# Optimization experiments

Hardware: AMD Instinct MI355X
Metric: run time of the kernel (lower is better)

Reference implementation:

```python
import jax, jax.numpy as jnp
import numpy as np

B, N, DIM = 4, 2048, 768
HEADS, DH, DEPTH = 12, 64, 4
W = 35                     # hard-coded window size
P = DIM // 2               # window-embedding proj dim
V4 = DIM // 4              # window-embedding value dim
PB = DIM // 4              # dynamic pos-bias MLP width
FF = DIM * 4
NEG = float(np.finfo(np.float32).max)


def setup_inputs() -> dict:
    key = jax.random.key(0)
    ks = iter(jax.random.split(key, 32))
    r = lambda shape: jax.random.normal(next(ks), shape, jnp.float32) * 0.02
    return dict(
        x=jax.random.normal(next(ks), (B, N, DIM), jnp.float32),
        mask=jnp.zeros((B, N), bool),
        ln1_g=jnp.ones((DEPTH, DIM)), ln1_b=jnp.zeros((DEPTH, DIM)),
        qkv_W=r((DEPTH, DIM, 3 * HEADS * DH)),
        temp=jnp.full((DEPTH,), 15.5, jnp.float32),
        we_lin_W=r((DEPTH, DIM, P)), we_q_W=r((DEPTH, P, P)),
        we_k_W=r((DEPTH, DIM, P)), we_v_W=r((DEPTH, DIM, V4)),
        we_bos=jnp.zeros((DEPTH, V4)), we_scale=jnp.ones((DEPTH,)),
        out_W=r((DEPTH, DIM + V4, DIM)),
        ln2_g=jnp.ones((DEPTH, DIM)), ln2_b=jnp.zeros((DEPTH, DIM)),
        glu_W=r((DEPTH, DIM, 2 * FF)), glu_b=jnp.zeros((DEPTH, 2 * FF)),
        ffo_W=r((DEPTH, FF, DIM)), ffo_b=jnp.zeros((DEPTH, DIM)),
        pb_W1=r((1, PB)), pb_b1=jnp.zeros((PB,)),
        pb_W2=r((PB, PB)), pb_b2=jnp.zeros((PB,)),
        pb_W3=r((PB, HEADS)), pb_b3=jnp.zeros((HEADS,)),
    )


def _ln(x, g, b):
    m = x.mean(-1, keepdims=True)
    v = ((x - m) ** 2).mean(-1, keepdims=True)
    return (x - m) * jax.lax.rsqrt(v + 1e-5) * g + b


def _l2norm(t):
    # matches F.normalize(p=2, dim=-1): x / max(||x||, 1e-12)
    return t / jnp.maximum(jnp.linalg.norm(t, axis=-1, keepdims=True), 1e-12)


def _pos_bias(n, W1, b1, W2, b2, W3, b3):
    # DynamicPositionBias(dim=PB, depth=2): Linear->ReLU, Linear->ReLU, Linear
    pos = jnp.arange(-n + 1, n, dtype=jnp.float32)[:, None]          # (2n-1, 1)
    h = jax.nn.relu(pos @ W1 + b1)
    h = jax.nn.relu(h @ W2 + b2)
    out = h @ W3 + b3                                                # (2n-1, H)
    idx = jnp.arange(n)[:, None] - jnp.arange(n)[None, :] + n - 1    # (n, n)
    return jnp.transpose(out[idx], (2, 0, 1))                        # (H, n, n)


def _sinu(n, scale):
    # ScaledSinuEmbedding over proj dim P
    inv = 1.0 / (10000.0 ** (jnp.arange(0, P, 2, dtype=jnp.float32) / P))
    s = jnp.arange(n, dtype=jnp.float32)[:, None] * inv[None, :]
    return jnp.concatenate([jnp.sin(s), jnp.cos(s)], -1) * scale     # (n, P)


def _forward(x, mask, ln1_g, ln1_b, qkv_W, temp, we_lin_W, we_q_W, we_k_W,
             we_v_W, we_bos, we_scale, out_W, ln2_g, ln2_b, glu_W, glu_b,
             ffo_W, ffo_b, pb_W1, pb_b1, pb_W2, pb_b2, pb_W3, pb_b3):
    Bz, Nn, _ = x.shape
    pad = (-Nn) % W
    nw = (Nn + pad) // W
    bias = _pos_bias(W, pb_W1, pb_b1, pb_W2, pb_b2, pb_W3, pb_b3)    # (H, W, W)
    causal = jnp.triu(jnp.ones((W, W), bool), 1)
    mpad = jnp.concatenate([mask, jnp.ones((Bz, pad), bool)], 1).reshape(Bz, nw, W)
    valid = ~mpad                                                    # (B, w, n)
    amask = ~(valid[:, None, :, :, None] & valid[:, None, :, None, :]) | causal
    we_mask = mpad[:, :, None, :]                                    # (B, w, 1, n)
    lengths = jnp.maximum(valid.sum(-1), 1).astype(jnp.float32)[..., None, None]
    sinu35 = _sinu(W, 1.0)                                           # (W, P)

    for l in range(DEPTH):
        # ---- PreNorm + windowed cosine attention ----
        h = _ln(x, ln1_g[l], ln1_b[l])
        hp = jnp.concatenate([h, jnp.zeros((Bz, pad, DIM), h.dtype)], 1)
        hp = hp.reshape(Bz, nw, W, DIM)
        qkv = (hp @ qkv_W[l]).reshape(Bz, nw, W, HEADS, DH, 3)
        q, k, v = (jnp.transpose(qkv[..., i], (0, 3, 1, 2, 4)) for i in range(3))
        q, k = _l2norm(q), _l2norm(k)
        dots = jnp.einsum('bhwid,bhwjd->bhwij', q, k) * temp[l] + bias[None, :, None]
        dots = jnp.where(amask, -NEG, dots)
        attn = jax.nn.softmax(dots, axis=-1)
        o = jnp.einsum('bhwij,bhwjd->bhwid', attn, v)
        o = jnp.transpose(o, (0, 2, 3, 1, 4)).reshape(Bz, nw, W, HEADS * DH)
        # ---- window_embeddings: pooled prev-window embedding attention ----
        we = jnp.where(mpad[..., None], 0.0, o) @ we_lin_W[l]         # (B,w,n,P)
        we = jax.nn.relu(we.sum(-2, keepdims=True) / lengths)        # (B,w,1,P)
        wq = we @ we_q_W[l]
        k2 = o @ we_k_W[l] + sinu35 * we_scale[l]
        v2 = o @ we_v_W[l]
        d2 = jnp.einsum('bwid,bwjd->bwij', wq, k2) * (P ** -0.5)
        d2 = jnp.where(we_mask, -NEG, d2)
        o2 = jnp.einsum('bwij,bwjd->bwid', jax.nn.softmax(d2, -1), v2)  # (B,w,1,V4)
        bos = jnp.broadcast_to(we_bos[l], (Bz, 1, 1, V4))
        o2 = jnp.concatenate([bos, o2], 1)[:, :-1]                   # shift by one window
        o = jnp.concatenate([o, jnp.broadcast_to(o2, (Bz, nw, W, V4))], -1)
        o = (o @ out_W[l]).reshape(Bz, nw * W, DIM)[:, :Nn]
        x = x + o
        # ---- PreNorm + GLU feed-forward ----
        h2 = _ln(x, ln2_g[l], ln2_b[l])
        a, g = jnp.split(h2 @ glu_W[l] + glu_b[l], 2, axis=-1)
        x = x + ((a * jax.nn.silu(g)) @ ffo_W[l] + ffo_b[l])
    return x


def reference(x, mask, ln1_g, ln1_b, qkv_W, temp, we_lin_W, we_q_W, we_k_W,
              we_v_W, we_bos, we_scale, out_W, ln2_g, ln2_b, glu_W, glu_b,
              ffo_W, ffo_b, pb_W1, pb_b1, pb_W2, pb_b2, pb_W3, pb_b3):
    return _forward(x, mask, ln1_g, ln1_b, qkv_W, temp, we_lin_W, we_q_W,
                    we_k_W, we_v_W, we_bos, we_scale, out_W, ln2_g, ln2_b,
                    glu_W, glu_b, ffo_W, ffo_b, pb_W1, pb_b1, pb_W2, pb_b2,
                    pb_W3, pb_b3)
```

## Files before the change

### kernel.cpp

```cpp
#include <hip/hip_runtime.h>
#include <hip/hip_bf16.h>
#include <cstddef>
#include <cstdint>

#define B_ 4
#define N_ 2048
#define DIM_ 768
#define HEADS_ 12
#define DH_ 64
#define DEPTH_ 4
#define W_ 35
#define P_ 384
#define V4_ 192
#define FF_ 3072
#define NW_ 59
#define NPB_ (NW_*W_)
#define NTOK_ (B_*N_)
#define NWB_ (B_*NW_)
#define NTP_ (NWB_*W_)
#define NTPA_ 8448
#define NEG_ 3.402823466e+38f
#define QLD_ 65

typedef __bf16 bf16x8 __attribute__((ext_vector_type(8)));
typedef float  f32x4  __attribute__((ext_vector_type(4)));

#define GLOAD16(g, l) __builtin_amdgcn_global_load_lds( \
    (const __attribute__((address_space(1))) uint32_t*)(g), \
    (__attribute__((address_space(3))) uint32_t*)(l), 16, 0, 0)


__global__ __launch_bounds__(192) void posbias1_k(
    const float* __restrict__ W1, const float* __restrict__ b1,
    const float* __restrict__ W2, const float* __restrict__ b2,
    const float* __restrict__ W3, const float* __restrict__ b3,
    float* __restrict__ outk)
{
    __shared__ float h1[192];
    __shared__ float h2[192];
    int i = blockIdx.x;
    int tid = threadIdx.x;
    float pos = (float)(i - 34);
    h1[tid] = fmaxf(pos*W1[tid] + b1[tid], 0.f);
    __syncthreads();
    float s = b2[tid];
    for (int k=0;k<192;k++) s += h1[k]*W2[k*192+tid];
    h2[tid] = fmaxf(s, 0.f);
    __syncthreads();
    if (tid < 12){
        float o = b3[tid];
        for (int k=0;k<192;k++) o += h2[k]*W3[k*12+tid];
        outk[i*12+tid] = o;
    }
}

__global__ void posbias2_k(const float* __restrict__ outk, float* __restrict__ bias)
{
    int e = threadIdx.x + blockIdx.x*blockDim.x;
    if (e >= HEADS_*W_*W_) return;
    int h=e/(W_*W_); int rem=e%(W_*W_); int i=rem/W_; int j=rem%W_;
    bias[e] = outk[(i-j+W_-1)*12 + h];
}

__global__ void sinu_k(float* __restrict__ sinu)
{
    int i = blockIdx.x;
    int k = threadIdx.x;
    float inv = powf(10000.f, -(float)k/192.f);
    float s = (float)i * inv;
    sinu[i*P_ + k]       = sinf(s);
    sinu[i*P_ + 192 + k] = cosf(s);
}

__global__ void len_k(const unsigned char* __restrict__ mask, float* __restrict__ len)
{
    int bw = threadIdx.x + blockIdx.x*blockDim.x;
    if (bw >= NWB_) return;
    int b = bw / NW_, w = bw % NW_;
    int cnt = 0;
    for (int t=0;t<W_;t++){
        int g = w*W_ + t;
        if (g < N_ && mask[b*N_+g]==0) cnt++;
    }
    len[bw] = fmaxf((float)cnt, 1.f);
}

__global__ __launch_bounds__(256) void bosproj_k(
    const float* __restrict__ bos, const float* __restrict__ outW,
    float* __restrict__ bosp)
{
    int l = blockIdx.y;
    int c = blockIdx.x*256 + threadIdx.x;
    if (c >= DIM_) return;
    const float* W2 = outW + (size_t)l*(DIM_+V4_)*DIM_ + (size_t)DIM_*DIM_;
    const float* bl = bos + (size_t)l*V4_;
    float s = 0;
    for (int k=0;k<V4_;k++) s += bl[k]*W2[(size_t)k*DIM_ + c];
    bosp[(size_t)l*DIM_ + c] = s;
}

__global__ __launch_bounds__(256) void pack_k(
    const float* __restrict__ W, __bf16* __restrict__ Bp,
    int N, int Ncov, int Nld, size_t lsW, size_t lsB, int qkvperm, int ncol0)
{
    int n = blockIdx.x*256 + threadIdx.x;
    int k8 = blockIdx.y, l = blockIdx.z;
    if (n >= Ncov) return;
    bf16x8 v;
    if (n < N){
        int sn = n;
        if (qkvperm){ int s = n/768, hd = n - s*768; sn = hd*3 + s; }
        const float* w = W + lsW*l + (size_t)k8*8*N + sn;
        #pragma unroll
        for (int e=0;e<8;e++) v[e] = (__bf16)w[(size_t)e*N];
    } else {
        #pragma unroll
        for (int e=0;e<8;e++) v[e] = (__bf16)0.f;
    }
    *(bf16x8*)(Bp + lsB*l + ((size_t)k8*Nld + ncol0 + n)*8) = v;
}

__global__ __launch_bounds__(256) void ln_k(
    const float* __restrict__ x, const float* __restrict__ g,
    const float* __restrict__ b, __bf16* __restrict__ out,
    const float* __restrict__ o2p, const float* __restrict__ bosp, int padded)
{
    int r = blockIdx.x;
    int tid = threadIdx.x;
    int lane = tid & 63, wave = tid >> 6;
    int row = r; bool real = true;
    if (padded){
        int bb = r / NPB_, n = r % NPB_;
        if (n >= N_) real = false;
        row = bb*N_ + n;
    }
    float v0=0,v1=0,v2=0;
    if (real){
        const float* xr = x + (size_t)row*DIM_;
        v0 = xr[tid]; v1 = xr[tid+256]; v2 = xr[tid+512];
        if (o2p){
            int bb = row / N_, nn = row % N_;
            int widx = nn / W_;
            const float* op = widx ? o2p + (size_t)(bb*NW_ + widx - 1)*DIM_
                                   : bosp;
            v0 += op[tid]; v1 += op[tid+256]; v2 += op[tid+512];
        }
    }
    float s1 = v0+v1+v2;
    float s2 = v0*v0+v1*v1+v2*v2;
    #pragma unroll
    for (int off=32; off; off>>=1){
        s1 += __shfl_xor(s1, off);
        s2 += __shfl_xor(s2, off);
    }
    __shared__ float a1[4], a2[4];
    if (lane==0){ a1[wave]=s1; a2[wave]=s2; }
    __syncthreads();
    s1 = a1[0]+a1[1]+a1[2]+a1[3];
    s2 = a2[0]+a2[1]+a2[2]+a2[3];
    float m   = s1 * (1.f/768.f);
    float var = s2 * (1.f/768.f) - m*m;
    float inv = rsqrtf(var + 1e-5f);
    __bf16* o = out + (size_t)r*DIM_;
    if (!real){ o[tid]=(__bf16)0.f; o[tid+256]=(__bf16)0.f; o[tid+512]=(__bf16)0.f; return; }
    o[tid]     = (__bf16)((v0-m)*inv*g[tid]     + b[tid]);
    o[tid+256] = (__bf16)((v1-m)*inv*g[tid+256] + b[tid+256]);
    o[tid+512] = (__bf16)((v2-m)*inv*g[tid+512] + b[tid+512]);
}

template<int EPI, bool DUAL, int BM>
__global__ __launch_bounds__(256) void mgemm_k(
    const __bf16* __restrict__ A, const __bf16* __restrict__ Bp,
    float* __restrict__ Cf, __bf16* __restrict__ Cb, float* __restrict__ Cf2,
    float* __restrict__ Cx,
    const float* __restrict__ bias, const float* __restrict__ extra,
    const float* __restrict__ scale_ptr,
    int M, int K, int Nc, int Nld, int Cld)
{
    constexpr int BN = DUAL ? 64 : 128;
    constexpr int RS = BM / 2;
    constexpr int MF = RS / 16;
    constexpr int NF = (BN/2) / 16;
    constexpr int AS = BM * 32;
    constexpr int BS = BN * 32;
    constexpr int ALD = BM / 64;
    constexpr int NL  = ALD + 2;
    __shared__ alignas(16) __bf16 As[3*AS];
    __shared__ alignas(16) __bf16 Bs[3*BS];
    __shared__ alignas(16) __bf16 Gs[DUAL ? 3*BS : 16];
    const int tid = threadIdx.x;
    const int lane = tid & 63, wave = tid >> 6;
    const int wr = wave >> 1, wc = wave & 1;
    const int m0 = blockIdx.y*BM;
    const int n0 = blockIdx.x*BN;
    const int lk = lane >> 4, lr = lane & 15;
    f32x4 acc[MF][NF] = {};
    f32x4 acc2[DUAL?MF:1][NF] = {};

    const __bf16* aP[ALD];
    int aO[ALD];
    #pragma unroll
    for (int q=0;q<ALD;q++){
        int i = tid + q*256;
        int r = i & (BM-1), k8 = i / BM;
        aP[q] = A + (size_t)(m0+r)*K + k8*8;
        aO[q] = i*8;
    }
    const __bf16* bP[2];
    int bO[2];
    if constexpr (!DUAL){
        #pragma unroll
        for (int q=0;q<2;q++){
            int i = tid + q*256;
            int n = i & 127, k8 = i >> 7;
            bP[q] = Bp + ((size_t)k8*Nld + n0 + n)*8;
            bO[q] = i*8;
        }
    } else {
        int n = tid & 63, k8 = tid >> 6;
        bP[0] = Bp + ((size_t)k8*Nld + n0 + n)*8;
        bP[1] = bP[0] + (size_t)FF_*8;
        bO[0] = tid*8;
        bO[1] = tid*8;
    }
    const size_t bStep = (size_t)Nld*32;

    auto stage = [&](int wb){
        #pragma unroll
        for (int q=0;q<ALD;q++)
            GLOAD16(aP[q], As + wb*AS + aO[q]);
        if constexpr (!DUAL){
            GLOAD16(bP[0], Bs + wb*BS + bO[0]);
            GLOAD16(bP[1], Bs + wb*BS + bO[1]);
        } else {
            GLOAD16(bP[0], Bs + wb*BS + bO[0]);
            GLOAD16(bP[1], Gs + wb*BS + bO[1]);
        }
        #pragma unroll
        for (int q=0;q<ALD;q++) aP[q] += 32;
        bP[0] += bStep; bP[1] += bStep;
    };

    const int nk = K >> 5;
    stage(0);
    stage(1);
    int rb = 0;
    for (int t = 0; t < nk; ++t){
        if (t == nk-1)              asm volatile("s_waitcnt vmcnt(0)" ::: "memory");
        else if constexpr (NL == 3) asm volatile("s_waitcnt vmcnt(3)" ::: "memory");
        else                        asm volatile("s_waitcnt vmcnt(4)" ::: "memory");
        __builtin_amdgcn_s_barrier();
        __builtin_amdgcn_sched_barrier(0);
        if (t + 2 < nk){
            int wb = rb + 2; if (wb >= 3) wb -= 3;
            stage(wb);
        }
        const __bf16* as = As + rb*AS + (size_t)(lk*BM + wr*RS + lr)*8;
        const __bf16* bs = Bs + rb*BS + (size_t)(lk*BN + wc*(BN/2) + lr)*8;
        bf16x8 af[MF], bfr[NF];
        #pragma unroll
        for (int m=0;m<MF;m++) af[m] = *(const bf16x8*)(as + m*128);
        #pragma unroll
        for (int n=0;n<NF;n++) bfr[n] = *(const bf16x8*)(bs + n*128);
        __builtin_amdgcn_s_setprio(1);
        #pragma unroll
        for (int m=0;m<MF;m++)
            #pragma unroll
            for (int n=0;n<NF;n++)
                acc[m][n] = __builtin_amdgcn_mfma_f32_16x16x32_bf16(af[m], bfr[n], acc[m][n], 0,0,0);
        if constexpr (DUAL){
            const __bf16* gs = Gs + rb*BS + (size_t)(lk*BN + wc*(BN/2) + lr)*8;
            bf16x8 gfr[NF];
            #pragma unroll
            for (int n=0;n<NF;n++) gfr[n] = *(const bf16x8*)(gs + n*128);
            #pragma unroll
            for (int m=0;m<MF;m++)
                #pragma unroll
                for (int n=0;n<NF;n++)
                    acc2[m][n] = __builtin_amdgcn_mfma_f32_16x16x32_bf16(af[m], gfr[n], acc2[m][n], 0,0,0);
        }
        __builtin_amdgcn_s_setprio(0);
        rb++; if (rb >= 3) rb = 0;
    }

    const int lq = lane >> 4;
    #pragma unroll
    for (int m=0;m<MF;m++){
        #pragma unroll
        for (int r=0;r<4;r++){
            int row = m0 + wr*RS + m*16 + lq*4 + r;
            if (row >= M) continue;
            #pragma unroll
            for (int n=0;n<NF;n++){
                int col = n0 + wc*(BN/2) + n*16 + lr;
                if (col >= Nc) continue;
                float v = acc[m][n][r];
                if (EPI==1){
                    Cb[(size_t)row*Cld + col] = (__bf16)v;
                } else if (EPI==3){
                    int bb = row / N_, nn = row % N_;
                    int widx = nn / W_;
                    const float* src = widx
                        ? extra + (size_t)(bb*NW_ + widx - 1)*DIM_
                        : scale_ptr;
                    Cf[(size_t)row*Cld + col] += v + bias[col] + src[col];
                } else if (EPI==4){
                    float a_ = v + bias[col];
                    float g_ = acc2[m][n][r] + bias[col + FF_];
                    Cb[(size_t)row*Cld + col] = (__bf16)(a_ * (g_ / (1.f + expf(-g_))));
                } else if (EPI==8){
                    if (col < P_){
                        int tt = (row % NPB_) % W_;
                        Cf[(size_t)row*P_ + col] = v + extra[tt*P_ + col]*scale_ptr[0];
                    } else if (col < 576){
                        Cf2[(size_t)row*V4_ + (col - P_)] = v;
                    } else {
                        int bb = row / NPB_, nn = row % NPB_;
                        if (nn < N_)
                            Cx[(size_t)(bb*N_ + nn)*DIM_ + (col - 576)] += v;
                    }
                }
            }
        }
    }
}

__global__ __launch_bounds__(256) void attn_k(
    const __bf16* __restrict__ qkv, const unsigned char* __restrict__ mask,
    const float* __restrict__ bias, const float* __restrict__ temp_p,
    __bf16* __restrict__ obuf, float* __restrict__ osum)
{
    int bid = blockIdx.x;
    int w = bid % NW_;
    int h = (bid / NW_) % HEADS_;
    int b = bid / (NW_*HEADS_);
    int tid = threadIdx.x;
    __shared__ float qs[W_*QLD_], ks[W_*QLD_], vs[W_*DH_];
    __shared__ float sc[W_*W_];
    __shared__ float osacc[4][64];
    __shared__ int vf[W_];
    int bw = b*NW_ + w;
    int rbase = bw*W_;
    for (int e=tid; e<W_*DH_; e+=256){
        int t=e>>6, d=e&63;
        size_t idx = (size_t)(rbase+t)*(3*DIM_) + h*DH_ + d;
        qs[t*QLD_+d]=(float)qkv[idx];
        ks[t*QLD_+d]=(float)qkv[idx+768];
        vs[e]=(float)qkv[idx+1536];
    }
    if (tid < W_){
        int g = w*W_ + tid;
        vf[tid] = (g < N_) && (mask[b*N_+g]==0);
    }
    __syncthreads();
    for (int e=tid; e<2*W_; e+=256){
        float* src = (e<W_)? qs : ks;
        int t = (e<W_)? e : e-W_;
        float s=0;
        for (int d=0;d<DH_;d++){ float v=src[t*QLD_+d]; s+=v*v; }
        float inv = 1.f / fmaxf(sqrtf(s), 1e-12f);
        for (int d=0;d<DH_;d++) src[t*QLD_+d] *= inv;
    }
    __syncthreads();
    float temp = temp_p[0];
    for (int e=tid; e<W_*W_; e+=256){
        int i=e/W_, j=e%W_;
        float s;
        if (!vf[i] || !vf[j] || j>i) s = -NEG_;
        else {
            float acc=0;
            for (int d=0;d<DH_;d++) acc += qs[i*QLD_+d]*ks[j*QLD_+d];
            s = acc*temp + bias[(h*W_+i)*W_+j];
        }
        sc[e]=s;
    }
    __syncthreads();
    if (tid < W_){
        int i=tid;
        float mx=-INFINITY;
        for (int j=0;j<W_;j++) mx=fmaxf(mx, sc[i*W_+j]);
        float sum=0;
        for (int j=0;j<W_;j++){ float e_=expf(sc[i*W_+j]-mx); sc[i*W_+j]=e_; sum+=e_; }
        float inv=1.f/sum;
        for (int j=0;j<W_;j++) sc[i*W_+j]*=inv;
    }
    __syncthreads();
    int wavei = tid >> 6, d = tid & 63;
    float psum = 0.f;
    for (int i = wavei; i < W_; i += 4){
        float s=0;
        for (int j=0;j<W_;j++) s += sc[i*W_+j]*vs[j*DH_+d];
        obuf[(size_t)(rbase+i)*DIM_ + h*DH_ + d] = (__bf16)s;
        if (vf[i]) psum += s;
    }
    osacc[wavei][d] = psum;
    __syncthreads();
    if (tid < 64)
        osum[(size_t)bw*DIM_ + h*DH_ + tid] =
            osacc[0][tid]+osacc[1][tid]+osacc[2][tid]+osacc[3][tid];
}

__global__ __launch_bounds__(384) void wefuse_k(
    const float* __restrict__ osum, const float* __restrict__ we_lin,
    const float* __restrict__ we_q, const float* __restrict__ k2,
    const float* __restrict__ v2, const unsigned char* __restrict__ mask,
    const float* __restrict__ len, const float* __restrict__ W2,
    float* __restrict__ o2p)
{
    int bw = blockIdx.x;
    int b = bw / NW_, w = bw % NW_;
    int tid = threadIdx.x;
    __shared__ float osr[768], werr[384], wqr[384], pp[W_], o2s[V4_];
    osr[tid]     = osum[(size_t)bw*DIM_ + tid];
    osr[tid+384] = osum[(size_t)bw*DIM_ + tid + 384];
    __syncthreads();
    float invlen = 1.f / len[bw];
    float s = 0;
    for (int k=0;k<768;k++) s += osr[k]*we_lin[(size_t)k*P_ + tid];
    werr[tid] = fmaxf(s*invlen, 0.f);
    __syncthreads();
    s = 0;
    for (int k=0;k<384;k++) s += werr[k]*we_q[(size_t)k*P_ + tid];
    wqr[tid] = s;
    __syncthreads();
    if (tid < W_){
        int g = w*W_ + tid;
        bool val = (g < N_) && (mask[b*N_+g]==0);
        float sv = -NEG_;
        if (val){
            float acc=0;
            const float* kr = k2 + (size_t)(bw*W_+tid)*P_;
            for (int c=0;c<P_;c++) acc += wqr[c]*kr[c];
            sv = acc * 0.05103103630798287f;
        }
        pp[tid]=sv;
    }
    __syncthreads();
    if (tid==0){
        float mx=-INFINITY;
        for (int j=0;j<W_;j++) mx=fmaxf(mx,pp[j]);
        float sum=0;
        for (int j=0;j<W_;j++){ float e=expf(pp[j]-mx); pp[j]=e; sum+=e; }
        float inv=1.f/sum;
        for (int j=0;j<W_;j++) pp[j]*=inv;
    }
    __syncthreads();
    if (tid < V4_){
        float sv=0;
        for (int j=0;j<W_;j++) sv += pp[j]*v2[(size_t)(bw*W_+j)*V4_ + tid];
        o2s[tid] = sv;
    }
    __syncthreads();
    #pragma unroll
    for (int c = tid; c < DIM_; c += 384){
        float s2 = 0;
        for (int k=0;k<V4_;k++) s2 += o2s[k]*W2[(size_t)k*DIM_ + c];
        o2p[(size_t)bw*DIM_ + c] = s2;
    }
}


extern "C" void kernel_launch(void* const* d_in, const int* in_sizes, int n_in,
                              void* d_out, int out_size, void* d_ws, size_t ws_size,
                              hipStream_t stream)
{
    const float* x       = (const float*)d_in[0];
    const unsigned char* mask = (const unsigned char*)d_in[1];
    const float* ln1_g   = (const float*)d_in[2];
    const float* ln1_b   = (const float*)d_in[3];
    const float* qkv_W   = (const float*)d_in[4];
    const float* temp    = (const float*)d_in[5];
    const float* we_lin_W= (const float*)d_in[6];
    const float* we_q_W  = (const float*)d_in[7];
    const float* we_k_W  = (const float*)d_in[8];
    const float* we_v_W  = (const float*)d_in[9];
    const float* we_bos  = (const float*)d_in[10];
    const float* we_scale= (const float*)d_in[11];
    const float* out_W   = (const float*)d_in[12];
    const float* ln2_g   = (const float*)d_in[13];
    const float* ln2_b   = (const float*)d_in[14];
    const float* glu_W   = (const float*)d_in[15];
    const float* glu_b   = (const float*)d_in[16];
    const float* ffo_W   = (const float*)d_in[17];
    const float* ffo_b   = (const float*)d_in[18];
    const float* pb_W1   = (const float*)d_in[19];
    const float* pb_b1   = (const float*)d_in[20];
    const float* pb_W2   = (const float*)d_in[21];
    const float* pb_b2   = (const float*)d_in[22];
    const float* pb_W3   = (const float*)d_in[23];
    const float* pb_b3   = (const float*)d_in[24];

    float* xc = (float*)d_out;

    char* p = (char*)d_ws;
    auto alloc = [&](size_t bytes)->char* {
        char* r = p; p += (bytes + 255) & ~(size_t)255; return r;
    };
    float* f_outk = (float*)alloc((size_t)69*12*4);
    float* f_bias = (float*)alloc((size_t)HEADS_*W_*W_*4);
    float* f_sinu = (float*)alloc((size_t)W_*P_*4);
    float* f_len  = (float*)alloc((size_t)NWB_*4);
    float* f_osum = (float*)alloc((size_t)NWB_*DIM_*4);
    float* f_o2p  = (float*)alloc((size_t)NWB_*DIM_*4);
    float* f_bosp = (float*)alloc((size_t)DEPTH_*DIM_*4);
    __bf16* w_qkv = (__bf16*)alloc((size_t)DEPTH_*96*2304*8*2);
    __bf16* w_kvo = (__bf16*)alloc((size_t)DEPTH_*96*1408*8*2);
    __bf16* w_glu = (__bf16*)alloc((size_t)DEPTH_*96*6144*8*2);
    __bf16* w_ffo = (__bf16*)alloc((size_t)DEPTH_*384*768*8*2);
    char* arena = p;
    __bf16* f_hpad = (__bf16*)alloc((size_t)NTPA_*DIM_*2);
    __bf16* f_qkvb = (__bf16*)alloc((size_t)NTP_*3*DIM_*2);
    __bf16* f_obuf = (__bf16*)alloc((size_t)NTPA_*DIM_*2);
    float*  f_k2   = (float*)alloc((size_t)NTP_*P_*4);
    float*  f_v2   = (float*)alloc((size_t)NTP_*V4_*4);
    __bf16* f_h2 = (__bf16*)arena;
    __bf16* f_ag = (__bf16*)(arena + (((size_t)NTOK_*DIM_*2 + 255) & ~(size_t)255));
    (void)ws_size; (void)in_sizes; (void)n_in; (void)out_size;

    hipMemcpyAsync(xc, x, (size_t)NTOK_*DIM_*sizeof(float),
                   hipMemcpyDeviceToDevice, stream);
    posbias1_k<<<69,192,0,stream>>>(pb_W1,pb_b1,pb_W2,pb_b2,pb_W3,pb_b3,f_outk);
    posbias2_k<<<(HEADS_*W_*W_+255)/256,256,0,stream>>>(f_outk, f_bias);
    sinu_k<<<W_,192,0,stream>>>(f_sinu);
    len_k<<<1,256,0,stream>>>(mask, f_len);
    bosproj_k<<<dim3(3,DEPTH_),256,0,stream>>>(we_bos, out_W, f_bosp);
    pack_k<<<dim3(9,96,DEPTH_),256,0,stream>>>(qkv_W, w_qkv, 2304, 2304, 2304,
        (size_t)768*2304, (size_t)96*2304*8, 1, 0);
    pack_k<<<dim3(2,96,DEPTH_),256,0,stream>>>(we_k_W, w_kvo, 384, 384, 1408,
        (size_t)768*384, (size_t)96*1408*8, 0, 0);
    pack_k<<<dim3(1,96,DEPTH_),256,0,stream>>>(we_v_W, w_kvo, 192, 192, 1408,
        (size_t)768*192, (size_t)96*1408*8, 0, 384);
    pack_k<<<dim3(4,96,DEPTH_),256,0,stream>>>(out_W, w_kvo, 768, 832, 1408,
        (size_t)960*768, (size_t)96*1408*8, 0, 576);
    pack_k<<<dim3(24,96,DEPTH_),256,0,stream>>>(glu_W, w_glu, 6144, 6144, 6144,
        (size_t)768*6144, (size_t)96*6144*8, 0, 0);
    pack_k<<<dim3(3,384,DEPTH_),256,0,stream>>>(ffo_W, w_ffo, 768, 768, 768,
        (size_t)3072*768, (size_t)384*768*8, 0, 0);

    for (int l=0;l<DEPTH_;l++){
        const float* bosp_l = f_bosp + (size_t)l*DIM_;
        ln_k<<<NTP_,256,0,stream>>>(xc, ln1_g+l*DIM_, ln1_b+l*DIM_, f_hpad,
            nullptr, nullptr, 1);
        mgemm_k<1,false,128><<<dim3(18,65),256,0,stream>>>(f_hpad,
            w_qkv + (size_t)l*96*2304*8, nullptr, f_qkvb, nullptr, nullptr,
            nullptr, nullptr, nullptr, NTP_, DIM_, 3*DIM_, 3*DIM_, 3*DIM_);
        attn_k<<<B_*HEADS_*NW_,256,0,stream>>>(f_qkvb, mask, f_bias, temp+l,
            f_obuf, f_osum);
        mgemm_k<8,false,64><<<dim3(11,130),256,0,stream>>>(f_obuf,
            w_kvo + (size_t)l*96*1408*8, f_k2, nullptr, f_v2, xc,
            nullptr, f_sinu, we_scale+l, NTP_, DIM_, 1344, 1408, 0);
        wefuse_k<<<NWB_,384,0,stream>>>(f_osum, we_lin_W + (size_t)l*DIM_*P_,
            we_q_W + (size_t)l*P_*P_, f_k2, f_v2, mask, f_len,
            out_W + (size_t)l*(DIM_+V4_)*DIM_ + (size_t)DIM_*DIM_, f_o2p);

        ln_k<<<NTOK_,256,0,stream>>>(xc, ln2_g+l*DIM_, ln2_b+l*DIM_, f_h2,
            f_o2p, bosp_l, 0);
        mgemm_k<4,true,128><<<dim3(48,64),256,0,stream>>>(f_h2,
            w_glu + (size_t)l*96*6144*8, nullptr, f_ag, nullptr, nullptr,
            glu_b + (size_t)l*2*FF_, nullptr, nullptr,
            NTOK_, DIM_, FF_, 2*FF_, FF_);
        mgemm_k<3,false,64><<<dim3(6,128),256,0,stream>>>(f_ag,
            w_ffo + (size_t)l*384*768*8, xc, nullptr, nullptr, nullptr,
            ffo_b + (size_t)l*DIM_, f_o2p, bosp_l,
            NTOK_, FF_, DIM_, DIM_, DIM_);
    }
}
```

Measured before the change: 2.026 ms.

## Add dedicated 256x256 eight-wave GLU GEMM kernel with interleaved weight packing

Replaces the generic mgemm GLU launch with a specialized 512-thread kernel that computes 256x256 output tiles using double-buffered async LDS staging, split into quarter stages interleaved with MFMA compute and priority hints. The GLU weight pack gets a new permutation mode that interleaves value and gate columns so each wave holds matching a/g accumulators for the fused SiLU-gate epilogue. Larger tiles raise arithmetic intensity and reduce global traffic. The cost is high LDS use (128KB) and register pressure from 32 accumulator fragments, which limits occupancy.

```diff
diff --git a/kernel.cpp b/kernel.cpp
--- a/kernel.cpp
+++ b/kernel.cpp
@@ -101,7 +101,7 @@
 
 __global__ __launch_bounds__(256) void pack_k(
     const float* __restrict__ W, __bf16* __restrict__ Bp,
-    int N, int Ncov, int Nld, size_t lsW, size_t lsB, int qkvperm, int ncol0)
+    int N, int Ncov, int Nld, size_t lsW, size_t lsB, int mode, int ncol0)
 {
     int n = blockIdx.x*256 + threadIdx.x;
     int k8 = blockIdx.y, l = blockIdx.z;
@@ -109,7 +109,13 @@
     bf16x8 v;
     if (n < N){
         int sn = n;
-        if (qkvperm){ int s = n/768, hd = n - s*768; sn = hd*3 + s; }
+        if (mode == 1){ int s = n/768, hd = n - s*768; sn = hd*3 + s; }
+        else if (mode == 2){
+            int bx = n >> 8, c = n & 255;
+            int wcq = c >> 6, n2 = (c & 63) >> 4, lr2 = c & 15;
+            int j = bx*128 + wcq*32 + ((n2>>1)<<4) + lr2;
+            sn = (n2 & 1) ? FF_ + j : j;
+        }
         const float* w = W + lsW*l + (size_t)k8*8*N + sn;
         #pragma unroll
         for (int e=0;e<8;e++) v[e] = (__bf16)w[(size_t)e*N];
@@ -325,6 +331,119 @@
     }
 }
 
+__global__ __launch_bounds__(512) void glu8_k(
+    const __bf16* __restrict__ A, const __bf16* __restrict__ Bp,
+    __bf16* __restrict__ Cb, const float* __restrict__ bias)
+{
+    __shared__ alignas(16) __bf16 As[2][16384];
+    __shared__ alignas(16) __bf16 Bs[2][16384];
+    const int tid = threadIdx.x;
+    const int lane = tid & 63, wave = tid >> 6;
+    const int wr = wave >> 2, wc = wave & 3;
+    const int m0 = blockIdx.y << 8;
+    const int n0p = blockIdx.x << 8;
+    const int lk = lane >> 4, lr = lane & 15;
+    f32x4 acc[8][4] = {};
+
+    auto stageA = [&](int buf, int kt, int h){
+        #pragma unroll
+        for (int q=0;q<2;q++){
+            int i = tid + q*512;
+            int k8 = i >> 7, r = i & 127;
+            GLOAD16(A + (size_t)(m0 + h*128 + r)*DIM_ + kt*64 + k8*8,
+                    &As[buf][((size_t)k8*256 + h*128 + r)*8]);
+        }
+    };
+    auto stageB = [&](int buf, int kt, int h){
+        #pragma unroll
+        for (int q=0;q<2;q++){
+            int i = tid + q*512;
+            int k8 = i >> 7, c = i & 127;
+            GLOAD16(Bp + ((size_t)(kt*8 + k8)*6144 + n0p + h*128 + c)*8,
+                    &Bs[buf][((size_t)k8*256 + h*128 + c)*8]);
+        }
+    };
+    auto stageHalf = [&](int buf, int kt, int h){
+        if (h < 2) stageA(buf, kt, h); else stageB(buf, kt, h-2);
+    };
+
+    #pragma unroll
+    for (int h=0;h<4;h++) stageHalf(0, 0, h);
+    #pragma unroll
+    for (int h=0;h<4;h++) stageHalf(1, 1, h);
+    asm volatile("s_waitcnt vmcnt(8)" ::: "memory");
+    __builtin_amdgcn_s_barrier();
+    __builtin_amdgcn_sched_barrier(0);
+
+    const int niter = (DIM_/64) / 2;
+    for (int j = 0; j < niter; ++j){
+        #pragma unroll
+        for (int p = 0; p < 8; ++p){
+            const int g = p >> 2;
+            const int q = p & 3;
+            if (p == 0){
+                if (j > 0) asm volatile("s_waitcnt vmcnt(0)" ::: "memory");
+            } else if (p == 4){
+                asm volatile("s_waitcnt vmcnt(0)" ::: "memory");
+            }
+            if (g == 0){
+                if (j >= 1) stageHalf(1, 2*j+1, q);
+            } else {
+                if (2*j+2 < DIM_/64) stageHalf(0, 2*j+2, q);
+            }
+            const int rbase = wr*128 + (q&1)*64;
+            const int cbase = wc*64  + ((q>>1))*32;
+            const __bf16* as = &As[g][0];
+            const __bf16* bs = &Bs[g][0];
+            bf16x8 af[2][4], bfr[2][2];
+            #pragma unroll
+            for (int s=0;s<2;s++){
+                #pragma unroll
+                for (int m=0;m<4;m++)
+                    af[s][m] = *(const bf16x8*)(as + ((size_t)((s*4+lk)*256 + rbase + m*16 + lr))*8);
+                #pragma unroll
+                for (int n=0;n<2;n++)
+                    bfr[s][n] = *(const bf16x8*)(bs + ((size_t)((s*4+lk)*256 + cbase + n*16 + lr))*8);
+            }
+            __builtin_amdgcn_s_barrier();
+            __builtin_amdgcn_sched_barrier(0);
+            __builtin_amdgcn_s_setprio(1);
+            #pragma unroll
+            for (int s=0;s<2;s++)
+                #pragma unroll
+                for (int m=0;m<4;m++)
+                    #pragma unroll
+                    for (int n=0;n<2;n++)
+                        acc[(q&1)*4 + m][(q>>1)*2 + n] =
+                            __builtin_amdgcn_mfma_f32_16x16x32_bf16(
+                                af[s][m], bfr[s][n],
+                                acc[(q&1)*4 + m][(q>>1)*2 + n], 0,0,0);
+            __builtin_amdgcn_s_setprio(0);
+            __builtin_amdgcn_s_barrier();
+            __builtin_amdgcn_sched_barrier(0);
+        }
+    }
+
+    const int lq = lane >> 4;
+    const int jc0 = (blockIdx.x << 7) + wc*32 + lr;
+    #pragma unroll
+    for (int mm=0;mm<8;mm++){
+        int rowb = m0 + wr*128 + mm*16 + lq*4;
+        #pragma unroll
+        for (int hh=0; hh<2; hh++){
+            int col = jc0 + hh*16;
+            float ba = bias[col], bg = bias[col + FF_];
+            #pragma unroll
+            for (int r=0;r<4;r++){
+                float a_ = acc[mm][hh*2][r] + ba;
+                float g_ = acc[mm][hh*2+1][r] + bg;
+                Cb[(size_t)(rowb + r)*FF_ + col] =
+                    (__bf16)(a_ * (g_/(1.f + expf(-g_))));
+            }
+        }
+    }
+}
+
 __global__ __launch_bounds__(256) void attn_k(
     const __bf16* __restrict__ qkv, const unsigned char* __restrict__ mask,
     const float* __restrict__ bias, const float* __restrict__ temp_p,
@@ -533,7 +652,7 @@
     pack_k<<<dim3(4,96,DEPTH_),256,0,stream>>>(out_W, w_kvo, 768, 832, 1408,
         (size_t)960*768, (size_t)96*1408*8, 0, 576);
     pack_k<<<dim3(24,96,DEPTH_),256,0,stream>>>(glu_W, w_glu, 6144, 6144, 6144,
-        (size_t)768*6144, (size_t)96*6144*8, 0, 0);
+        (size_t)768*6144, (size_t)96*6144*8, 2, 0);
     pack_k<<<dim3(3,384,DEPTH_),256,0,stream>>>(ffo_W, w_ffo, 768, 768, 768,
         (size_t)3072*768, (size_t)384*768*8, 0, 0);
 
@@ -555,10 +674,8 @@
 
         ln_k<<<NTOK_,256,0,stream>>>(xc, ln2_g+l*DIM_, ln2_b+l*DIM_, f_h2,
             f_o2p, bosp_l, 0);
-        mgemm_k<4,true,128><<<dim3(48,64),256,0,stream>>>(f_h2,
-            w_glu + (size_t)l*96*6144*8, nullptr, f_ag, nullptr, nullptr,
-            glu_b + (size_t)l*2*FF_, nullptr, nullptr,
-            NTOK_, DIM_, FF_, 2*FF_, FF_);
+        glu8_k<<<dim3(24,32),512,0,stream>>>(f_h2,
+            w_glu + (size_t)l*96*6144*8, f_ag, glu_b + (size_t)l*2*FF_);
         mgemm_k<3,false,64><<<dim3(6,128),256,0,stream>>>(f_ag,
             w_ffo + (size_t)l*384*768*8, xc, nullptr, nullptr, nullptr,
             ffo_b + (size_t)l*DIM_, f_o2p, bosp_l,
```

Measured after the change: 1.987 ms. Within noise of the previous version (-1.9%).
